# Performance work log

Hardware: AMD Instinct MI355X
Metric: run time of the kernel (lower is better)

The kernel has to match this reference:

```python
import jax, jax.numpy as jnp
import numpy as np

B, T, D, S = 64, 512, 1024, 1024


def setup_inputs() -> dict:
    key = jax.random.key(0)
    k1, k2, k3, k4 = jax.random.split(key, 4)
    a = jax.random.normal(k1, (B, T, D), dtype=jnp.float32)
    s_prev = jax.random.normal(k2, (B, S), dtype=jnp.float32)
    # Dense(10, tanh) over concat dim D+S; Dense(1, relu). Glorot-ish scale.
    W1 = jax.random.normal(k3, (D + S, 10), dtype=jnp.float32) * (1.0 / np.sqrt(D + S))
    b1 = jnp.zeros((10,), dtype=jnp.float32)
    W2 = jax.random.normal(k4, (10, 1), dtype=jnp.float32) * (1.0 / np.sqrt(10))
    b2 = jnp.zeros((1,), dtype=jnp.float32)
    return {"a": a, "s_prev": s_prev, "W1": W1, "b1": b1, "W2": W2, "b2": b2}


def reference(a, s_prev, W1, b1, W2, b2):
    # RepeatVector: [B,S] -> [B,T,S]
    s_rep = jnp.broadcast_to(s_prev[:, None, :], (a.shape[0], a.shape[1], s_prev.shape[-1]))
    x = jnp.concatenate([a, s_rep], axis=-1)               # [B,T,D+S]
    h = jnp.tanh(jnp.einsum('btc,cu->btu', x, W1) + b1)    # [B,T,10]
    e = jax.nn.relu(jnp.einsum('btu,uo->bto', h, W2) + b2) # [B,T,1]
    attention_score = jax.nn.softmax(e, axis=1)            # softmax over time
    context_vector = jnp.sum(attention_score * a, axis=1, keepdims=True)  # [B,1,D]
    return context_vector, attention_score
```

## Files before the change

### kernel.cpp

```cpp
#include <hip/hip_runtime.h>

#define B_ 64
#define T_ 512
#define D_ 1024
#define S_ 1024
#define U_ 10

typedef float f32x2 __attribute__((ext_vector_type(2)));
typedef float f32x4 __attribute__((ext_vector_type(4)));

static constexpr int WS_PMZ = 0;
static constexpr int WS_E   = 1024;
static constexpr int WS_PV  = 33792;

template <int CTRL>
__device__ __forceinline__ float dpp_add(float x) {
    int yi = __builtin_amdgcn_update_dpp(0, __float_as_int(x), CTRL, 0xf, 0xf, true);
    return x + __int_as_float(yi);
}

__device__ __forceinline__ float wave_sum_uniform(float x) {
    x = dpp_add<0x111>(x);
    x = dpp_add<0x112>(x);
    x = dpp_add<0x114>(x);
    x = dpp_add<0x118>(x);
    x = dpp_add<0x142>(x);
    x = dpp_add<0x143>(x);
    return __int_as_float(__builtin_amdgcn_readlane(__float_as_int(x), 63));
}

__device__ __forceinline__ float uload(const float* p) {
    return __int_as_float(__builtin_amdgcn_readfirstlane(__float_as_int(*p)));
}
__device__ __forceinline__ float uniformf(float x) {
    return __int_as_float(__builtin_amdgcn_readfirstlane(__float_as_int(x)));
}

__device__ __forceinline__ f32x2 pk_fma(f32x2 a, f32x2 b, f32x2 c) {
#if __has_builtin(__builtin_elementwise_fma)
    return __builtin_elementwise_fma(a, b, c);
#else
    return a * b + c;
#endif
}

__global__ __launch_bounds__(256, 2) void k1_main(const float* __restrict__ a,
                                                  const float* __restrict__ s_prev,
                                                  const float* __restrict__ W1,
                                                  const float* __restrict__ b1,
                                                  const float* __restrict__ W2,
                                                  const float* __restrict__ b2,
                                                  float* __restrict__ ws) {
    const int blk  = blockIdx.x;
    const int b    = blk >> 3;
    const int p    = blk & 7;
    const int tid  = threadIdx.x;
    const int wave = tid >> 6;
    const int lane = tid & 63;

    float c[U_];
    {
        float cacc[U_];
#pragma unroll
        for (int u = 0; u < U_; u++) cacc[u] = 0.f;
#pragma unroll
        for (int r = 0; r < 4; r++) {
            const f32x4 s4 = *(const f32x4*)(s_prev + b * S_ + r * 256 + lane * 4);
            const float svv[4] = {s4.x, s4.y, s4.z, s4.w};
#pragma unroll
            for (int i = 0; i < 4; i++) {
                const int s = r * 256 + lane * 4 + i;
                const float* wp = W1 + (size_t)(D_ + s) * U_;
#pragma unroll
                for (int h = 0; h < 5; h++) {
                    f32x2 t = *(const f32x2*)(wp + 2 * h);
                    cacc[2 * h]     += svv[i] * t.x;
                    cacc[2 * h + 1] += svv[i] * t.y;
                }
            }
        }
#pragma unroll
        for (int u = 0; u < U_; u++)
            c[u] = uniformf(wave_sum_uniform(cacc[u]) + uload(b1 + u));
    }

    float w2v[U_];
#pragma unroll
    for (int u = 0; u < U_; u++) w2v[u] = uload(W2 + u);
    const float b2s = uload(b2);

    f32x2 w1p[4][2][U_];
#pragma unroll
    for (int k = 0; k < 4; k++) {
        const float* wp = W1 + (size_t)(k * 256 + lane * 4) * U_;
        float wbuf[40];
#pragma unroll
        for (int q = 0; q < 10; q++) {
            f32x4 t = *(const f32x4*)(wp + 4 * q);
            wbuf[4 * q + 0] = t.x; wbuf[4 * q + 1] = t.y;
            wbuf[4 * q + 2] = t.z; wbuf[4 * q + 3] = t.w;
        }
#pragma unroll
        for (int u = 0; u < U_; u++) {
            w1p[k][0][u] = f32x2{wbuf[u],      wbuf[10 + u]};
            w1p[k][1][u] = f32x2{wbuf[20 + u], wbuf[30 + u]};
        }
    }

    f32x2 v2[4][2];
#pragma unroll
    for (int k = 0; k < 4; k++) { v2[k][0] = 0.f; v2[k][1] = 0.f; }
    float m = -1e30f, Z = 0.f;

    const int t0 = p * 64 + wave * 16;
    const float* abase = a + ((size_t)(b * T_ + t0)) * D_ + lane * 4;

    f32x4 bufA[4], bufB[4];
#pragma unroll
    for (int k = 0; k < 4; k++) bufA[k] = *(const f32x4*)(abase + k * 256);

    auto calc_e = [&](const f32x4* buf) -> float {
        f32x2 acc2[U_];
#pragma unroll
        for (int u = 0; u < U_; u++) acc2[u] = 0.f;
#pragma unroll
        for (int k = 0; k < 4; k++) {
            const f32x2 alo = buf[k].lo;
            const f32x2 ahi = buf[k].hi;
#pragma unroll
            for (int u = 0; u < U_; u++) {
                acc2[u] = pk_fma(alo, w1p[k][0][u], acc2[u]);
                acc2[u] = pk_fma(ahi, w1p[k][1][u], acc2[u]);
            }
        }
        float tm[U_];
#pragma unroll
        for (int u = 0; u < U_; u++) {
            float s = wave_sum_uniform(acc2[u].x + acc2[u].y);
            float x = s + c[u];
            float ex = exp2f(x * 2.8853900817779268f);
            float th = 1.f - 2.f * __builtin_amdgcn_rcpf(ex + 1.f);
            tm[u] = th * w2v[u];
        }
        float e = ((tm[0] + tm[1]) + (tm[2] + tm[3])) +
                  ((tm[4] + tm[5]) + (tm[6] + tm[7])) +
                  ((tm[8] + tm[9]) + b2s);
        return fmaxf(e, 0.f);
    };

    auto step = [&](const f32x4* buf, int tt) {
        float e = calc_e(buf);
        if (lane == 0) ws[WS_E + b * T_ + t0 + tt] = e;
        if (e > m) {
            float sc = exp2f((m - e) * 1.4426950408889634f);
            Z = Z * sc + 1.f;
            f32x2 scv = {sc, sc};
#pragma unroll
            for (int k = 0; k < 4; k++) {
                v2[k][0] = pk_fma(v2[k][0], scv, buf[k].lo);
                v2[k][1] = pk_fma(v2[k][1], scv, buf[k].hi);
            }
            m = e;
        } else {
            float w = exp2f((e - m) * 1.4426950408889634f);
            Z += w;
            f32x2 wv = {w, w};
#pragma unroll
            for (int k = 0; k < 4; k++) {
                v2[k][0] = pk_fma(wv, buf[k].lo, v2[k][0]);
                v2[k][1] = pk_fma(wv, buf[k].hi, v2[k][1]);
            }
        }
    };

#pragma unroll 1
    for (int tt = 0; tt < 16; tt += 2) {
        const float* apB = abase + (size_t)(tt + 1) * D_;
#pragma unroll
        for (int k = 0; k < 4; k++) bufB[k] = *(const f32x4*)(apB + k * 256);
        step(bufA, tt);
        if (tt < 14) {
            const float* apA = abase + (size_t)(tt + 2) * D_;
#pragma unroll
            for (int k = 0; k < 4; k++) bufA[k] = *(const f32x4*)(apA + k * 256);
        }
        step(bufB, tt + 1);
    }

    __shared__ f32x4 vs4[4][256];
    __shared__ float mzs[4][2];
#pragma unroll
    for (int k = 0; k < 4; k++) {
        f32x4 o;
        o.lo = v2[k][0];
        o.hi = v2[k][1];
        vs4[wave][k * 64 + lane] = o;
    }
    if (lane == 0) { mzs[wave][0] = m; mzs[wave][1] = Z; }
    __syncthreads();

    float m0 = mzs[0][0], m1 = mzs[1][0], m2 = mzs[2][0], m3 = mzs[3][0];
    float mb = fmaxf(fmaxf(m0, m1), fmaxf(m2, m3));
    float f0 = __expf(m0 - mb), f1 = __expf(m1 - mb);
    float f2 = __expf(m2 - mb), f3 = __expf(m3 - mb);
    float Zb = f0 * mzs[0][1] + f1 * mzs[1][1] + f2 * mzs[2][1] + f3 * mzs[3][1];

    f32x4 t0v = vs4[0][tid], t1v = vs4[1][tid], t2v = vs4[2][tid], t3v = vs4[3][tid];
    f32x4 o = f0 * t0v + f1 * t1v + f2 * t2v + f3 * t3v;
    ((f32x4*)(ws + WS_PV))[blk * 256 + tid] = o;
    if (tid == 0) { ws[WS_PMZ + blk * 2] = mb; ws[WS_PMZ + blk * 2 + 1] = Zb; }
}

__global__ __launch_bounds__(256) void k2_final(const float* __restrict__ ws,
                                                float* __restrict__ out) {
    const int b = blockIdx.x;
    const int tid = threadIdx.x;

    float pm[8], pz[8];
    float mb = -1e30f;
#pragma unroll
    for (int p = 0; p < 8; p++) {
        pm[p] = ws[WS_PMZ + (b * 8 + p) * 2];
        pz[p] = ws[WS_PMZ + (b * 8 + p) * 2 + 1];
        mb = fmaxf(mb, pm[p]);
    }
    float f[8], Z = 0.f;
#pragma unroll
    for (int p = 0; p < 8; p++) { f[p] = __expf(pm[p] - mb); Z += f[p] * pz[p]; }
    const float rz = 1.f / Z;

    float4 o = make_float4(0.f, 0.f, 0.f, 0.f);
#pragma unroll
    for (int p = 0; p < 8; p++) {
        float4 t = ((const float4*)(ws + WS_PV))[(b * 8 + p) * 256 + tid];
        o.x += f[p] * t.x; o.y += f[p] * t.y; o.z += f[p] * t.z; o.w += f[p] * t.w;
    }
    o.x *= rz; o.y *= rz; o.z *= rz; o.w *= rz;
    ((float4*)out)[b * 256 + tid] = o;

    for (int t = tid; t < T_; t += 256) {
        out[B_ * D_ + b * T_ + t] = __expf(ws[WS_E + b * T_ + t] - mb) * rz;
    }
}

extern "C" void kernel_launch(void* const* d_in, const int* in_sizes, int n_in,
                              void* d_out, int out_size, void* d_ws, size_t ws_size,
                              hipStream_t stream) {
    const float* a      = (const float*)d_in[0];
    const float* s_prev = (const float*)d_in[1];
    const float* W1     = (const float*)d_in[2];
    const float* b1     = (const float*)d_in[3];
    const float* W2     = (const float*)d_in[4];
    const float* b2     = (const float*)d_in[5];
    float* out = (float*)d_out;
    float* ws  = (float*)d_ws;

    k1_main<<<dim3(B_ * 8), dim3(256), 0, stream>>>(a, s_prev, W1, b1, W2, b2, ws);
    k2_final<<<dim3(B_), dim3(256), 0, stream>>>(ws, out);
}
```

Measured before the change: 212.0 us.

## Split each block's D across threads and process 16 timesteps per block

Each block now covers 16 timesteps, with every thread owning 4 of the D columns, instead of 64 timesteps per block with each wave owning 16. This gives 2048 blocks instead of 512. Per-wave partial dot products go to shared memory and are combined by 16 threads to compute e. The block then re-reads the same a rows to build the weighted context sum, so there is no cross-wave merge. The W1 register footprint shrinks, which allows 4 blocks per CU. In exchange, a is read twice per block (the second read may hit cache), the s_prev·W1 constant is recomputed in each of 4x more blocks, and k2 merges 32 partials per batch instead of 8.

New measurement: 234.1 us. +10.4%, slower.

```diff
diff --git a/kernel.cpp b/kernel.cpp
--- a/kernel.cpp
+++ b/kernel.cpp
@@ -5,13 +5,16 @@
 #define D_ 1024
 #define S_ 1024
 #define U_ 10
+#define CHUNKS_ 32
+#define TC_ 16
+#define NBLK_ (B_ * CHUNKS_)
 
 typedef float f32x2 __attribute__((ext_vector_type(2)));
 typedef float f32x4 __attribute__((ext_vector_type(4)));
 
 static constexpr int WS_PMZ = 0;
-static constexpr int WS_E   = 1024;
-static constexpr int WS_PV  = 33792;
+static constexpr int WS_E   = NBLK_ * 2;
+static constexpr int WS_PV  = WS_E + B_ * T_;
 
 template <int CTRL>
 __device__ __forceinline__ float dpp_add(float x) {
@@ -19,14 +22,18 @@
     return x + __int_as_float(yi);
 }
 
-__device__ __forceinline__ float wave_sum_uniform(float x) {
+__device__ __forceinline__ float wave_sum63(float x) {
     x = dpp_add<0x111>(x);
     x = dpp_add<0x112>(x);
     x = dpp_add<0x114>(x);
     x = dpp_add<0x118>(x);
     x = dpp_add<0x142>(x);
     x = dpp_add<0x143>(x);
-    return __int_as_float(__builtin_amdgcn_readlane(__float_as_int(x), 63));
+    return x;
+}
+
+__device__ __forceinline__ float wave_sum_uniform(float x) {
+    return __int_as_float(__builtin_amdgcn_readlane(__float_as_int(wave_sum63(x)), 63));
 }
 
 __device__ __forceinline__ float uload(const float* p) {
@@ -44,7 +51,7 @@
 #endif
 }
 
-__global__ __launch_bounds__(256, 2) void k1_main(const float* __restrict__ a,
+__global__ __launch_bounds__(256, 4) void k1_main(const float* __restrict__ a,
                                                   const float* __restrict__ s_prev,
                                                   const float* __restrict__ W1,
                                                   const float* __restrict__ b1,
@@ -52,14 +59,18 @@
                                                   const float* __restrict__ b2,
                                                   float* __restrict__ ws) {
     const int blk  = blockIdx.x;
-    const int b    = blk >> 3;
-    const int p    = blk & 7;
+    const int b    = blk >> 5;
+    const int p    = blk & 31;
     const int tid  = threadIdx.x;
     const int wave = tid >> 6;
     const int lane = tid & 63;
-
-    float c[U_];
-    {
+    const int d4   = tid * 4;
+
+    __shared__ float pmat[4][TC_][U_];
+    __shared__ __align__(16) float esh[TC_];
+
+    float c[U_], w2v[U_], b2s = 0.f;
+    if (wave == 0) {
         float cacc[U_];
 #pragma unroll
         for (int u = 0; u < U_; u++) cacc[u] = 0.f;
@@ -73,142 +84,143 @@
                 const float* wp = W1 + (size_t)(D_ + s) * U_;
 #pragma unroll
                 for (int h = 0; h < 5; h++) {
-                    f32x2 t = *(const f32x2*)(wp + 2 * h);
-                    cacc[2 * h]     += svv[i] * t.x;
-                    cacc[2 * h + 1] += svv[i] * t.y;
+                    f32x2 t2 = *(const f32x2*)(wp + 2 * h);
+                    cacc[2 * h]     += svv[i] * t2.x;
+                    cacc[2 * h + 1] += svv[i] * t2.y;
                 }
             }
         }
 #pragma unroll
         for (int u = 0; u < U_; u++)
             c[u] = uniformf(wave_sum_uniform(cacc[u]) + uload(b1 + u));
-    }
-
-    float w2v[U_];
-#pragma unroll
-    for (int u = 0; u < U_; u++) w2v[u] = uload(W2 + u);
-    const float b2s = uload(b2);
-
-    f32x2 w1p[4][2][U_];
-#pragma unroll
-    for (int k = 0; k < 4; k++) {
-        const float* wp = W1 + (size_t)(k * 256 + lane * 4) * U_;
-        float wbuf[40];
-#pragma unroll
-        for (int q = 0; q < 10; q++) {
-            f32x4 t = *(const f32x4*)(wp + 4 * q);
-            wbuf[4 * q + 0] = t.x; wbuf[4 * q + 1] = t.y;
-            wbuf[4 * q + 2] = t.z; wbuf[4 * q + 3] = t.w;
+#pragma unroll
+        for (int u = 0; u < U_; u++) w2v[u] = uload(W2 + u);
+        b2s = uload(b2);
+    }
+
+    f32x2 w1A[U_], w1B[U_];
+    {
+        float wbuf[4][U_];
+#pragma unroll
+        for (int i = 0; i < 4; i++) {
+            const float* wp = W1 + (size_t)(d4 + i) * U_;
+#pragma unroll
+            for (int h = 0; h < 5; h++) {
+                f32x2 t2 = *(const f32x2*)(wp + 2 * h);
+                wbuf[i][2 * h]     = t2.x;
+                wbuf[i][2 * h + 1] = t2.y;
+            }
         }
 #pragma unroll
         for (int u = 0; u < U_; u++) {
-            w1p[k][0][u] = f32x2{wbuf[u],      wbuf[10 + u]};
-            w1p[k][1][u] = f32x2{wbuf[20 + u], wbuf[30 + u]};
-        }
-    }
-
-    f32x2 v2[4][2];
-#pragma unroll
-    for (int k = 0; k < 4; k++) { v2[k][0] = 0.f; v2[k][1] = 0.f; }
-    float m = -1e30f, Z = 0.f;
-
-    const int t0 = p * 64 + wave * 16;
-    const float* abase = a + ((size_t)(b * T_ + t0)) * D_ + lane * 4;
-
-    f32x4 bufA[4], bufB[4];
-#pragma unroll
-    for (int k = 0; k < 4; k++) bufA[k] = *(const f32x4*)(abase + k * 256);
-
-    auto calc_e = [&](const f32x4* buf) -> float {
-        f32x2 acc2[U_];
-#pragma unroll
-        for (int u = 0; u < U_; u++) acc2[u] = 0.f;
-#pragma unroll
-        for (int k = 0; k < 4; k++) {
-            const f32x2 alo = buf[k].lo;
-            const f32x2 ahi = buf[k].hi;
-#pragma unroll
-            for (int u = 0; u < U_; u++) {
-                acc2[u] = pk_fma(alo, w1p[k][0][u], acc2[u]);
-                acc2[u] = pk_fma(ahi, w1p[k][1][u], acc2[u]);
-            }
-        }
-        float tm[U_];
+            w1A[u] = f32x2{wbuf[0][u], wbuf[1][u]};
+            w1B[u] = f32x2{wbuf[2][u], wbuf[3][u]};
+        }
+    }
+
+    const int t0 = p * TC_;
+    const float* abase = a + ((size_t)(b * T_ + t0)) * D_ + d4;
+
+    auto dot_step = [&](const f32x4 av, int t) {
+        f32x2 acc[U_];
+#pragma unroll
+        for (int u = 0; u < U_; u++)
+            acc[u] = pk_fma(av.hi, w1B[u], av.lo * w1A[u]);
+        float h[U_];
+#pragma unroll
+        for (int u = 0; u < U_; u++) h[u] = wave_sum63(acc[u].x + acc[u].y);
+        if (lane == 63) {
+#pragma unroll
+            for (int u = 0; u < U_; u++) pmat[wave][t][u] = h[u];
+        }
+    };
+
+    {
+        f32x4 av0 = *(const f32x4*)(abase + 0 * D_);
+        f32x4 av1 = *(const f32x4*)(abase + 1 * D_);
+        f32x4 av2 = *(const f32x4*)(abase + 2 * D_);
+        f32x4 av3 = *(const f32x4*)(abase + 3 * D_);
+#pragma unroll
+        for (int g = 0; g < 4; g++) {
+            dot_step(av0, 4 * g + 0);
+            if (g < 3) av0 = *(const f32x4*)(abase + (size_t)(4 * g + 4) * D_);
+            dot_step(av1, 4 * g + 1);
+            if (g < 3) av1 = *(const f32x4*)(abase + (size_t)(4 * g + 5) * D_);
+            dot_step(av2, 4 * g + 2);
+            if (g < 3) av2 = *(const f32x4*)(abase + (size_t)(4 * g + 6) * D_);
+            dot_step(av3, 4 * g + 3);
+            if (g < 3) av3 = *(const f32x4*)(abase + (size_t)(4 * g + 7) * D_);
+        }
+    }
+
+    __syncthreads();
+
+    if (tid < TC_) {
+        const int t = tid;
+        float e = b2s;
 #pragma unroll
         for (int u = 0; u < U_; u++) {
-            float s = wave_sum_uniform(acc2[u].x + acc2[u].y);
-            float x = s + c[u];
+            float x = pmat[0][t][u] + pmat[1][t][u] + pmat[2][t][u] + pmat[3][t][u] + c[u];
             float ex = exp2f(x * 2.8853900817779268f);
             float th = 1.f - 2.f * __builtin_amdgcn_rcpf(ex + 1.f);
-            tm[u] = th * w2v[u];
-        }
-        float e = ((tm[0] + tm[1]) + (tm[2] + tm[3])) +
-                  ((tm[4] + tm[5]) + (tm[6] + tm[7])) +
-                  ((tm[8] + tm[9]) + b2s);
-        return fmaxf(e, 0.f);
-    };
-
-    auto step = [&](const f32x4* buf, int tt) {
-        float e = calc_e(buf);
-        if (lane == 0) ws[WS_E + b * T_ + t0 + tt] = e;
+            e += th * w2v[u];
+        }
+        e = fmaxf(e, 0.f);
+        esh[t] = e;
+        ws[WS_E + b * T_ + t0 + t] = e;
+    }
+    __syncthreads();
+
+    const f32x4 e0 = *(const f32x4*)&esh[0];
+    const f32x4 e1 = *(const f32x4*)&esh[4];
+    const f32x4 e2 = *(const f32x4*)&esh[8];
+    const f32x4 e3 = *(const f32x4*)&esh[12];
+    const float ev[TC_] = {e0.x, e0.y, e0.z, e0.w, e1.x, e1.y, e1.z, e1.w,
+                           e2.x, e2.y, e2.z, e2.w, e3.x, e3.y, e3.z, e3.w};
+
+    float m = -1e30f, Z = 0.f;
+    f32x2 vlo = f32x2{0.f, 0.f}, vhi = f32x2{0.f, 0.f};
+
+    auto v_step = [&](const f32x4 av, float e) {
         if (e > m) {
             float sc = exp2f((m - e) * 1.4426950408889634f);
             Z = Z * sc + 1.f;
             f32x2 scv = {sc, sc};
-#pragma unroll
-            for (int k = 0; k < 4; k++) {
-                v2[k][0] = pk_fma(v2[k][0], scv, buf[k].lo);
-                v2[k][1] = pk_fma(v2[k][1], scv, buf[k].hi);
-            }
+            vlo = pk_fma(vlo, scv, av.lo);
+            vhi = pk_fma(vhi, scv, av.hi);
             m = e;
         } else {
             float w = exp2f((e - m) * 1.4426950408889634f);
             Z += w;
             f32x2 wv = {w, w};
-#pragma unroll
-            for (int k = 0; k < 4; k++) {
-                v2[k][0] = pk_fma(wv, buf[k].lo, v2[k][0]);
-                v2[k][1] = pk_fma(wv, buf[k].hi, v2[k][1]);
-            }
+            vlo = pk_fma(wv, av.lo, vlo);
+            vhi = pk_fma(wv, av.hi, vhi);
         }
     };
 
-#pragma unroll 1
-    for (int tt = 0; tt < 16; tt += 2) {
-        const float* apB = abase + (size_t)(tt + 1) * D_;
-#pragma unroll
-        for (int k = 0; k < 4; k++) bufB[k] = *(const f32x4*)(apB + k * 256);
-        step(bufA, tt);
-        if (tt < 14) {
-            const float* apA = abase + (size_t)(tt + 2) * D_;
-#pragma unroll
-            for (int k = 0; k < 4; k++) bufA[k] = *(const f32x4*)(apA + k * 256);
-        }
-        step(bufB, tt + 1);
-    }
-
-    __shared__ f32x4 vs4[4][256];
-    __shared__ float mzs[4][2];
-#pragma unroll
-    for (int k = 0; k < 4; k++) {
-        f32x4 o;
-        o.lo = v2[k][0];
-        o.hi = v2[k][1];
-        vs4[wave][k * 64 + lane] = o;
-    }
-    if (lane == 0) { mzs[wave][0] = m; mzs[wave][1] = Z; }
-    __syncthreads();
-
-    float m0 = mzs[0][0], m1 = mzs[1][0], m2 = mzs[2][0], m3 = mzs[3][0];
-    float mb = fmaxf(fmaxf(m0, m1), fmaxf(m2, m3));
-    float f0 = __expf(m0 - mb), f1 = __expf(m1 - mb);
-    float f2 = __expf(m2 - mb), f3 = __expf(m3 - mb);
-    float Zb = f0 * mzs[0][1] + f1 * mzs[1][1] + f2 * mzs[2][1] + f3 * mzs[3][1];
-
-    f32x4 t0v = vs4[0][tid], t1v = vs4[1][tid], t2v = vs4[2][tid], t3v = vs4[3][tid];
-    f32x4 o = f0 * t0v + f1 * t1v + f2 * t2v + f3 * t3v;
+    {
+        f32x4 av0 = *(const f32x4*)(abase + 0 * D_);
+        f32x4 av1 = *(const f32x4*)(abase + 1 * D_);
+        f32x4 av2 = *(const f32x4*)(abase + 2 * D_);
+        f32x4 av3 = *(const f32x4*)(abase + 3 * D_);
+#pragma unroll
+        for (int g = 0; g < 4; g++) {
+            v_step(av0, ev[4 * g + 0]);
+            if (g < 3) av0 = *(const f32x4*)(abase + (size_t)(4 * g + 4) * D_);
+            v_step(av1, ev[4 * g + 1]);
+            if (g < 3) av1 = *(const f32x4*)(abase + (size_t)(4 * g + 5) * D_);
+            v_step(av2, ev[4 * g + 2]);
+            if (g < 3) av2 = *(const f32x4*)(abase + (size_t)(4 * g + 6) * D_);
+            v_step(av3, ev[4 * g + 3]);
+            if (g < 3) av3 = *(const f32x4*)(abase + (size_t)(4 * g + 7) * D_);
+        }
+    }
+
+    f32x4 o;
+    o.lo = vlo;
+    o.hi = vhi;
     ((f32x4*)(ws + WS_PV))[blk * 256 + tid] = o;
-    if (tid == 0) { ws[WS_PMZ + blk * 2] = mb; ws[WS_PMZ + blk * 2 + 1] = Zb; }
+    if (tid == 0) { ws[WS_PMZ + blk * 2] = m; ws[WS_PMZ + blk * 2 + 1] = Z; }
 }
 
 __global__ __launch_bounds__(256) void k2_final(const float* __restrict__ ws,
@@ -216,27 +228,27 @@
     const int b = blockIdx.x;
     const int tid = threadIdx.x;
 
-    float pm[8], pz[8];
+    float pm[CHUNKS_], pz[CHUNKS_];
     float mb = -1e30f;
 #pragma unroll
-    for (int p = 0; p < 8; p++) {
-        pm[p] = ws[WS_PMZ + (b * 8 + p) * 2];
-        pz[p] = ws[WS_PMZ + (b * 8 + p) * 2 + 1];
+    for (int p = 0; p < CHUNKS_; p++) {
+        pm[p] = ws[WS_PMZ + (b * CHUNKS_ + p) * 2];
+        pz[p] = ws[WS_PMZ + (b * CHUNKS_ + p) * 2 + 1];
         mb = fmaxf(mb, pm[p]);
     }
-    float f[8], Z = 0.f;
-#pragma unroll
-    for (int p = 0; p < 8; p++) { f[p] = __expf(pm[p] - mb); Z += f[p] * pz[p]; }
+    float f[CHUNKS_], Z = 0.f;
+#pragma unroll
+    for (int p = 0; p < CHUNKS_; p++) { f[p] = __expf(pm[p] - mb); Z += f[p] * pz[p]; }
     const float rz = 1.f / Z;
 
-    float4 o = make_float4(0.f, 0.f, 0.f, 0.f);
-#pragma unroll
-    for (int p = 0; p < 8; p++) {
-        float4 t = ((const float4*)(ws + WS_PV))[(b * 8 + p) * 256 + tid];
-        o.x += f[p] * t.x; o.y += f[p] * t.y; o.z += f[p] * t.z; o.w += f[p] * t.w;
-    }
-    o.x *= rz; o.y *= rz; o.z *= rz; o.w *= rz;
-    ((float4*)out)[b * 256 + tid] = o;
+    f32x4 o = f32x4{0.f, 0.f, 0.f, 0.f};
+#pragma unroll
+    for (int p = 0; p < CHUNKS_; p++) {
+        f32x4 t = ((const f32x4*)(ws + WS_PV))[(b * CHUNKS_ + p) * 256 + tid];
+        o += f[p] * t;
+    }
+    o *= rz;
+    ((f32x4*)out)[b * 256 + tid] = o;
 
     for (int t = tid; t < T_; t += 256) {
         out[B_ * D_ + b * T_ + t] = __expf(ws[WS_E + b * T_ + t] - mb) * rz;
@@ -255,6 +267,6 @@
     float* out = (float*)d_out;
     float* ws  = (float*)d_ws;
 
-    k1_main<<<dim3(B_ * 8), dim3(256), 0, stream>>>(a, s_prev, W1, b1, W2, b2, ws);
+    k1_main<<<dim3(NBLK_), dim3(256), 0, stream>>>(a, s_prev, W1, b1, W2, b2, ws);
     k2_final<<<dim3(B_), dim3(256), 0, stream>>>(ws, out);
 }
```

## Stream activation rows through per-wave LDS ring with async global_load_lds

Applied to the files above, without the earlier changes.

Replaces the two-row register double buffer with a four-slot LDS ring per wave. Rows of `a` are filled by asynchronous `global_load_lds` transfers issued three rows ahead, and explicit `vmcnt` waits plus scheduling barriers gate each row's compute. The goal is to keep more memory requests in flight per wave and hide global-memory latency in this bandwidth-heavy reduction. The cost is 64 KB of LDS per block, which may limit occupancy, and an extra LDS read per row. The hand-counted `vmcnt` values also depend on how the lane-0 score stores are counted.

New measurement: 217.1 us. +2.4%, slower.

```diff
diff --git a/kernel.cpp b/kernel.cpp
--- a/kernel.cpp
+++ b/kernel.cpp
@@ -1,4 +1,5 @@
 #include <hip/hip_runtime.h>
+#include <stdint.h>
 
 #define B_ 64
 #define T_ 512
@@ -58,6 +59,9 @@
     const int wave = tid >> 6;
     const int lane = tid & 63;
 
+    __shared__ __align__(16) float stg[4][4][1024];
+    __shared__ float mzs[4][2];
+
     float c[U_];
     {
         float cacc[U_];
@@ -73,9 +77,9 @@
                 const float* wp = W1 + (size_t)(D_ + s) * U_;
 #pragma unroll
                 for (int h = 0; h < 5; h++) {
-                    f32x2 t = *(const f32x2*)(wp + 2 * h);
-                    cacc[2 * h]     += svv[i] * t.x;
-                    cacc[2 * h + 1] += svv[i] * t.y;
+                    f32x2 t2 = *(const f32x2*)(wp + 2 * h);
+                    cacc[2 * h]     += svv[i] * t2.x;
+                    cacc[2 * h + 1] += svv[i] * t2.y;
                 }
             }
         }
@@ -109,30 +113,46 @@
 
     f32x2 v2[4][2];
 #pragma unroll
-    for (int k = 0; k < 4; k++) { v2[k][0] = 0.f; v2[k][1] = 0.f; }
+    for (int k = 0; k < 4; k++) { v2[k][0] = f32x2{0.f, 0.f}; v2[k][1] = f32x2{0.f, 0.f}; }
     float m = -1e30f, Z = 0.f;
 
     const int t0 = p * 64 + wave * 16;
-    const float* abase = a + ((size_t)(b * T_ + t0)) * D_ + lane * 4;
-
-    f32x4 bufA[4], bufB[4];
-#pragma unroll
-    for (int k = 0; k < 4; k++) bufA[k] = *(const f32x4*)(abase + k * 256);
-
-    auto calc_e = [&](const f32x4* buf) -> float {
+    const size_t arow = (size_t)(b * T_ + t0) * D_;
+    const float* asrc = a + arow + lane * 4;
+
+    auto stage = [&](int tt) {
+        const int slot = tt & 3;
+        const float* src = asrc + (size_t)tt * D_;
+#pragma unroll
+        for (int k = 0; k < 4; k++) {
+            __builtin_amdgcn_global_load_lds(
+                (const __attribute__((address_space(1))) uint32_t*)(src + k * 256),
+                (__attribute__((address_space(3))) uint32_t*)&stg[wave][slot][k * 256],
+                16, 0, 0);
+        }
+    };
+
+    auto body = [&](int tt) {
+        const float* tb = &stg[wave][tt & 3][0];
+        f32x4 av[4];
+#pragma unroll
+        for (int k = 0; k < 4; k++)
+            av[k] = *(const f32x4*)(tb + k * 256 + lane * 4);
+
         f32x2 acc2[U_];
 #pragma unroll
-        for (int u = 0; u < U_; u++) acc2[u] = 0.f;
+        for (int u = 0; u < U_; u++) acc2[u] = f32x2{0.f, 0.f};
 #pragma unroll
         for (int k = 0; k < 4; k++) {
-            const f32x2 alo = buf[k].lo;
-            const f32x2 ahi = buf[k].hi;
+            const f32x2 alo = av[k].lo;
+            const f32x2 ahi = av[k].hi;
 #pragma unroll
             for (int u = 0; u < U_; u++) {
                 acc2[u] = pk_fma(alo, w1p[k][0][u], acc2[u]);
                 acc2[u] = pk_fma(ahi, w1p[k][1][u], acc2[u]);
             }
         }
+
         float tm[U_];
 #pragma unroll
         for (int u = 0; u < U_; u++) {
@@ -145,20 +165,17 @@
         float e = ((tm[0] + tm[1]) + (tm[2] + tm[3])) +
                   ((tm[4] + tm[5]) + (tm[6] + tm[7])) +
                   ((tm[8] + tm[9]) + b2s);
-        return fmaxf(e, 0.f);
-    };
-
-    auto step = [&](const f32x4* buf, int tt) {
-        float e = calc_e(buf);
+        e = fmaxf(e, 0.f);
         if (lane == 0) ws[WS_E + b * T_ + t0 + tt] = e;
+
         if (e > m) {
             float sc = exp2f((m - e) * 1.4426950408889634f);
             Z = Z * sc + 1.f;
             f32x2 scv = {sc, sc};
 #pragma unroll
             for (int k = 0; k < 4; k++) {
-                v2[k][0] = pk_fma(v2[k][0], scv, buf[k].lo);
-                v2[k][1] = pk_fma(v2[k][1], scv, buf[k].hi);
+                v2[k][0] = pk_fma(v2[k][0], scv, av[k].lo);
+                v2[k][1] = pk_fma(v2[k][1], scv, av[k].hi);
             }
             m = e;
         } else {
@@ -167,34 +184,39 @@
             f32x2 wv = {w, w};
 #pragma unroll
             for (int k = 0; k < 4; k++) {
-                v2[k][0] = pk_fma(wv, buf[k].lo, v2[k][0]);
-                v2[k][1] = pk_fma(wv, buf[k].hi, v2[k][1]);
+                v2[k][0] = pk_fma(wv, av[k].lo, v2[k][0]);
+                v2[k][1] = pk_fma(wv, av[k].hi, v2[k][1]);
             }
         }
     };
 
+    stage(0); stage(1); stage(2);
+
 #pragma unroll 1
-    for (int tt = 0; tt < 16; tt += 2) {
-        const float* apB = abase + (size_t)(tt + 1) * D_;
-#pragma unroll
-        for (int k = 0; k < 4; k++) bufB[k] = *(const f32x4*)(apB + k * 256);
-        step(bufA, tt);
-        if (tt < 14) {
-            const float* apA = abase + (size_t)(tt + 2) * D_;
-#pragma unroll
-            for (int k = 0; k < 4; k++) bufA[k] = *(const f32x4*)(apA + k * 256);
-        }
-        step(bufB, tt + 1);
-    }
-
-    __shared__ f32x4 vs4[4][256];
-    __shared__ float mzs[4][2];
+    for (int tt = 0; tt < 13; tt++) {
+        stage(tt + 3);
+        asm volatile("s_waitcnt vmcnt(12)" ::: "memory");
+        __builtin_amdgcn_sched_barrier(0);
+        body(tt);
+    }
+    asm volatile("s_waitcnt vmcnt(8)" ::: "memory");
+    __builtin_amdgcn_sched_barrier(0);
+    body(13);
+    asm volatile("s_waitcnt vmcnt(4)" ::: "memory");
+    __builtin_amdgcn_sched_barrier(0);
+    body(14);
+    asm volatile("s_waitcnt vmcnt(0)" ::: "memory");
+    __builtin_amdgcn_sched_barrier(0);
+    body(15);
+
+    __syncthreads();
+    f32x4* vs4 = (f32x4*)&stg[0][0][0];
 #pragma unroll
     for (int k = 0; k < 4; k++) {
         f32x4 o;
         o.lo = v2[k][0];
         o.hi = v2[k][1];
-        vs4[wave][k * 64 + lane] = o;
+        vs4[wave * 256 + k * 64 + lane] = o;
     }
     if (lane == 0) { mzs[wave][0] = m; mzs[wave][1] = Z; }
     __syncthreads();
@@ -205,7 +227,8 @@
     float f2 = __expf(m2 - mb), f3 = __expf(m3 - mb);
     float Zb = f0 * mzs[0][1] + f1 * mzs[1][1] + f2 * mzs[2][1] + f3 * mzs[3][1];
 
-    f32x4 t0v = vs4[0][tid], t1v = vs4[1][tid], t2v = vs4[2][tid], t3v = vs4[3][tid];
+    f32x4 t0v = vs4[0 * 256 + tid], t1v = vs4[1 * 256 + tid];
+    f32x4 t2v = vs4[2 * 256 + tid], t3v = vs4[3 * 256 + tid];
     f32x4 o = f0 * t0v + f1 * t1v + f2 * t2v + f3 * t3v;
     ((f32x4*)(ws + WS_PV))[blk * 256 + tid] = o;
     if (tid == 0) { ws[WS_PMZ + blk * 2] = mb; ws[WS_PMZ + blk * 2 + 1] = Zb; }
@@ -229,14 +252,14 @@
     for (int p = 0; p < 8; p++) { f[p] = __expf(pm[p] - mb); Z += f[p] * pz[p]; }
     const float rz = 1.f / Z;
 
-    float4 o = make_float4(0.f, 0.f, 0.f, 0.f);
+    f32x4 o = f32x4{0.f, 0.f, 0.f, 0.f};
 #pragma unroll
     for (int p = 0; p < 8; p++) {
-        float4 t = ((const float4*)(ws + WS_PV))[(b * 8 + p) * 256 + tid];
-        o.x += f[p] * t.x; o.y += f[p] * t.y; o.z += f[p] * t.z; o.w += f[p] * t.w;
-    }
-    o.x *= rz; o.y *= rz; o.z *= rz; o.w *= rz;
-    ((float4*)out)[b * 256 + tid] = o;
+        f32x4 t = ((const f32x4*)(ws + WS_PV))[(b * 8 + p) * 256 + tid];
+        o += f[p] * t;
+    }
+    o *= rz;
+    ((f32x4*)out)[b * 256 + tid] = o;
 
     for (int t = tid; t < T_; t += 256) {
         out[B_ * D_ + b * T_ + t] = __expf(ws[WS_E + b * T_ + t] - mb) * rz;
```
